# Performance work log

Hardware: AMD Instinct MI355X
Metric: run time of the kernel (lower is better)

## Reference

```python
import jax, jax.numpy as jnp
import numpy as np

IN_CH = 256
OUT_CH = 256
LATENT = 512
SCALE = 1.0 / IN_CH ** 0.5


def setup_inputs() -> dict:
    key = jax.random.key(0)
    k1, k2, k3, k4 = jax.random.split(key, 4)
    return {
        "x": jax.random.normal(k1, (16, IN_CH, 64, 64), dtype=jnp.float32),
        "w": jax.random.normal(k2, (16, LATENT), dtype=jnp.float32),
        "style_w": jax.random.normal(k3, (IN_CH, LATENT), dtype=jnp.float32) * (1.0 / LATENT ** 0.5),
        "style_b": jnp.zeros((IN_CH,), dtype=jnp.float32),
        "weight": jax.random.normal(k4, (1, OUT_CH, IN_CH, 3, 3), dtype=jnp.float32),
    }


def reference(x, w, style_w, style_b, weight):
    b, c, h, ws = x.shape
    # style = Linear(latent -> in_channels), reshaped to [b,1,in,1,1]
    style = (w @ style_w.T + style_b)[:, None, :, None, None]
    wt = weight * SCALE                    # [1, O, I, 3, 3]
    wt = wt * (style + 1.0)                # [b, O, I, 3, 3]
    demod = jax.lax.rsqrt(jnp.sum(wt * wt, axis=(2, 3, 4), keepdims=True) + 1e-8)
    wt = wt * demod
    # grouped conv: fold batch into channels, groups = b
    x2 = x.reshape(1, b * c, h, ws)
    k = wt.reshape(b * OUT_CH, c, 3, 3)
    out = jax.lax.conv_general_dilated(
        x2, k,
        window_strides=(1, 1),
        padding=((1, 1), (1, 1)),
        dimension_numbers=("NCHW", "OIHW", "NCHW"),
        feature_group_count=b,
    )
    return out.reshape(b, OUT_CH, h, ws)
```

## Files before the change

### kernel.cpp

```cpp
#include <hip/hip_runtime.h>
#include <hip/hip_bf16.h>

#define IN_CH 256
#define OUT_CH 256
#define LATENT 512
#define MSCALE (1.0f / 16.0f)

typedef __attribute__((ext_vector_type(8)))  short bf16x8;
typedef __attribute__((ext_vector_type(16))) float f32x16;
typedef unsigned short u16;

__device__ __forceinline__ u16 f2bf(float f) {
  unsigned int x = __float_as_uint(f);
  x += 0x7fffu + ((x >> 16) & 1u);
  return (u16)(x >> 16);
}

__device__ __forceinline__ void gload_lds16(const u16* g, u16* l) {
#if defined(__has_builtin) && __has_builtin(__builtin_amdgcn_global_load_lds)
  __builtin_amdgcn_global_load_lds(
      (const __attribute__((address_space(1))) unsigned int*)g,
      (__attribute__((address_space(3))) unsigned int*)l, 16, 0, 0);
#else
  int lane = __builtin_amdgcn_mbcnt_hi(~0u, __builtin_amdgcn_mbcnt_lo(~0u, 0));
  ((uint4*)l)[lane] = *(const uint4*)g;
#endif
}

__global__ void k_style_demod(const float* __restrict__ w, const float* __restrict__ sw,
                              const float* __restrict__ sb, const float* __restrict__ wsq,
                              float* __restrict__ mod, float* __restrict__ demod) {
  __shared__ float ws[LATENT];
  __shared__ float m2[IN_CH];
  const int b = blockIdx.x, tid = threadIdx.x;
  ws[tid] = w[b * LATENT + tid];
  ws[tid + 256] = w[b * LATENT + 256 + tid];
  __syncthreads();
  const float4* sr = (const float4*)(sw + (size_t)tid * LATENT);
  const float4* wr = (const float4*)ws;
  float s = 0.f;
#pragma unroll 8
  for (int l = 0; l < LATENT / 4; ++l) {
    float4 a = sr[l], c = wr[l];
    s += a.x * c.x + a.y * c.y + a.z * c.z + a.w * c.w;
  }
  float m = (1.0f + s + sb[tid]) * MSCALE;
  mod[b * IN_CH + tid] = m;
  m2[tid] = m * m;
  __syncthreads();
  float acc = 1e-8f;
  const float* q = wsq + (size_t)tid * IN_CH;
#pragma unroll 4
  for (int i = 0; i < IN_CH; ++i) acc += m2[i] * q[i];
  demod[b * OUT_CH + tid] = rsqrtf(acc);
}

__global__ void k_wsq(const float* __restrict__ weight, float* __restrict__ wsq,
                      u16* __restrict__ wb) {
  const int o = blockIdx.x, i = threadIdx.x;
  const float* wp = weight + ((size_t)o * IN_CH + i) * 9;
  float s = 0.f;
#pragma unroll
  for (int t = 0; t < 9; ++t) {
    float v = wp[t];
    s += v * v;
    wb[(((size_t)t * 32 + (i >> 3)) * OUT_CH + o) * 8 + (i & 7)] = f2bf(v);
  }
  wsq[o * IN_CH + i] = s;
}

__global__ __launch_bounds__(256, 2)
void k_conv(const float* __restrict__ x, const u16* __restrict__ wb,
            const float* __restrict__ mod, const float* __restrict__ demod,
            float* __restrict__ out) {
  __shared__ __align__(16) u16 xlds[2 * 10 * 2 * 66 * 8];
  __shared__ __align__(16) u16 wlds[2 * 9 * 2 * 64 * 8];
  __shared__ __align__(16) float modsh[IN_CH];

  const int tid = threadIdx.x;
  const int lane = tid & 63;
  const int wid = tid >> 6;
  const int ol = lane & 31;
  const int hi = lane >> 5;

  const int bid = blockIdx.x;
  const int sbid = ((bid & 7) << 6) | (bid >> 3);
  const int otile = (sbid & 3) << 6;
  const int hbase = ((sbid >> 2) & 7) << 3;
  const int b = sbid >> 5;

  const int sg = (tid >> 6) & 1;
  const int sc1 = tid & 63;
  const int rhalf = tid >> 7;
  const float* xb = x + (size_t)b * 1048576 + sg * 8 * 4096 + sc1;

  int woff[4];
#pragma unroll
  for (int it = 0; it < 4; ++it) {
    int p = it * 256 + tid;
    int t = p >> 7, g = (p >> 6) & 1, o = p & 63;
    woff[it] = ((t * 32 + g) * OUT_CH + otile + o) * 8;
  }
  const int wofft = ((8 * 32 + ((tid >> 6) & 1)) * OUT_CH + otile + (tid & 63)) * 8;

  float mv[8];
  auto ldmod = [&](int ib) {
    float4 m0 = *(const float4*)(modsh + ib + sg * 8);
    float4 m1 = *(const float4*)(modsh + ib + sg * 8 + 4);
    mv[0] = m0.x; mv[1] = m0.y; mv[2] = m0.z; mv[3] = m0.w;
    mv[4] = m1.x; mv[5] = m1.y; mv[6] = m1.z; mv[7] = m1.w;
  };
  auto issueX = [&](int k, int ib, float* v) {
    const int pr = hbase + 2 * k + rhalf;
    const int hc = min(max(pr - 1, 0), 63);
    const float* p = xb + hc * 64 + (size_t)ib * 4096;
#pragma unroll
    for (int j = 0; j < 8; ++j) v[j] = p[(size_t)j * 4096];
  };
  auto commitX = [&](int k, u16* xd, const float* v) {
    const int pr = hbase + 2 * k + rhalf;
    const bool vr = (pr >= 1) && (pr <= 64);
    bf16x8 q;
#pragma unroll
    for (int j = 0; j < 8; ++j) q[j] = vr ? (short)f2bf(v[j] * mv[j]) : (short)0;
    *(bf16x8*)(xd + (size_t)(((2 * k + rhalf) * 2 + sg) * 66 + sc1 + 1) * 8) = q;
  };
  auto stageW = [&](int ibw, u16* wd) {
#pragma unroll
    for (int it = 0; it < 4; ++it)
      gload_lds16(wb + woff[it] + ibw, wd + (size_t)(it * 256 + wid * 64) * 8);
    if (tid < 128)
      gload_lds16(wb + wofft + ibw, wd + (size_t)(1024 + wid * 64) * 8);
  };

  f32x16 acc[2][4] = {};

  modsh[tid] = mod[b * IN_CH + tid];
  if (tid < 80) {
    const int q = tid;
    const int bufz = q / 40, rem = q - bufz * 40;
    const int r = rem >> 2, g = (rem >> 1) & 1, ce = (rem & 1) * 65;
    bf16x8 z = {};
    *(bf16x8*)(xlds + (size_t)(bufz * 1320 + (r * 2 + g) * 66 + ce) * 8) = z;
  }
  __syncthreads();

  {
    float v0[8], v1[8];
    ldmod(0);
    stageW(0, wlds);
    issueX(0, 0, v0); issueX(1, 0, v1);
    commitX(0, xlds, v0); issueX(2, 0, v0);
    commitX(1, xlds, v1); issueX(3, 0, v1);
    commitX(2, xlds, v0); issueX(4, 0, v0);
    commitX(3, xlds, v1);
    commitX(4, xlds, v0);
  }
  __syncthreads();

  for (int ic = 0; ic < 16; ++ic) {
    const int buf = ic & 1;
    const u16* xp = xlds + buf * 10560;
    const u16* wp = wlds + buf * 9216;
    u16* xd = xlds + (buf ^ 1) * 10560;
    u16* wd = wlds + (buf ^ 1) * 9216;
    const bool pf = (ic < 15);
    const int ib = (ic + 1) << 4;

    float v0[8], v1[8];
    if (pf) {
      ldmod(ib);
      stageW((ic + 1) * 4096, wd);
      issueX(0, ib, v0);
      issueX(1, ib, v1);
    }

#pragma unroll
    for (int dh = 0; dh < 3; ++dh) {
      bf16x8 A0[3], A1[3];
#pragma unroll
      for (int dw = 0; dw < 3; ++dw) {
        const int t = dh * 3 + dw;
        A0[dw] = *(const bf16x8*)(wp + (size_t)((t * 2 + hi) * 64 + ol) * 8);
        A1[dw] = *(const bf16x8*)(wp + (size_t)((t * 2 + hi) * 64 + 32 + ol) * 8);
      }
      __builtin_amdgcn_s_setprio(1);
#pragma unroll
      for (int dw = 0; dw < 3; ++dw) {
#pragma unroll
        for (int ps = 0; ps < 4; ++ps) {
          const int r = 2 * wid + (ps >> 1) + dh;
          const int c = (ps & 1) * 32 + ol + dw;
          bf16x8 B = *(const bf16x8*)(xp + (size_t)((r * 2 + hi) * 66 + c) * 8);
          acc[0][ps] = __builtin_amdgcn_mfma_f32_32x32x16_bf16(A0[dw], B, acc[0][ps], 0, 0, 0);
          acc[1][ps] = __builtin_amdgcn_mfma_f32_32x32x16_bf16(A1[dw], B, acc[1][ps], 0, 0, 0);
        }
      }
      __builtin_amdgcn_s_setprio(0);
      if (pf) {
        if (dh == 0) {
          commitX(0, xd, v0); issueX(2, ib, v0);
          commitX(1, xd, v1); issueX(3, ib, v1);
        } else if (dh == 1) {
          commitX(2, xd, v0); issueX(4, ib, v0);
          commitX(3, xd, v1);
        } else {
          commitX(4, xd, v0);
        }
      }
    }
    __syncthreads();
  }

  const float* dmb = demod + b * OUT_CH + otile;
  float* outb = out + (size_t)b * OUT_CH * 4096;
#pragma unroll
  for (int os = 0; os < 2; ++os) {
    float dm[16];
#pragma unroll
    for (int qd = 0; qd < 4; ++qd) {
      float4 d4 = *(const float4*)(dmb + os * 32 + qd * 8 + hi * 4);
      dm[qd * 4 + 0] = d4.x; dm[qd * 4 + 1] = d4.y;
      dm[qd * 4 + 2] = d4.z; dm[qd * 4 + 3] = d4.w;
    }
#pragma unroll
    for (int ps = 0; ps < 4; ++ps) {
      const int prow = hbase + 2 * wid + (ps >> 1);
      const int col = (ps & 1) * 32 + ol;
#pragma unroll
      for (int rr = 0; rr < 16; ++rr) {
        const int orow = (rr & 3) + 8 * (rr >> 2) + 4 * hi;
        const int o = otile + os * 32 + orow;
        outb[(size_t)o * 4096 + prow * 64 + col] = acc[os][ps][rr] * dm[rr];
      }
    }
  }
}

extern "C" void kernel_launch(void* const* d_in, const int* in_sizes, int n_in,
                              void* d_out, int out_size, void* d_ws, size_t ws_size,
                              hipStream_t stream) {
  const float* x  = (const float*)d_in[0];
  const float* w  = (const float*)d_in[1];
  const float* sw = (const float*)d_in[2];
  const float* sb = (const float*)d_in[3];
  const float* wt = (const float*)d_in[4];
  float* out = (float*)d_out;

  char* ws = (char*)d_ws;
  u16*   wbuf  = (u16*)(ws);
  float* mod   = (float*)(ws + 1179648);
  float* demod = (float*)(ws + 1196032);
  float* wsq   = (float*)(ws + 1212416);
  if (ws_size < 1474560u) return;

  k_wsq        <<<256, 256, 0, stream>>>(wt, wsq, wbuf);
  k_style_demod<<<16, 256, 0, stream>>>(w, sw, sb, wsq, mod, demod);
  k_conv       <<<512, 256, 0, stream>>>(x, wbuf, mod, demod, out);
}
```

Before: 113.5 us.

## Merge prep kernels, compute demod in conv, batch x prefetch, packed bf16 convert

The two preprocessing kernels (weight square-sum and bf16 repack, plus the style linear) become one launch. The demodulation reduction moves into the conv kernel, where 64 threads compute it per block into shared memory. This removes a kernel launch and the serial dependency between them. The conv main loop now issues all five x row loads up front and commits them after the MFMA block, and uses the hardware packed bf16 convert instruction. Holding 40 prefetch floats per thread raises register pressure, which could limit occupancy. Each block also recomputes demod redundantly.

New measurement: 102.2 us. -10.0%, faster.

```diff
diff --git a/kernel.cpp b/kernel.cpp
--- a/kernel.cpp
+++ b/kernel.cpp
@@ -9,11 +9,18 @@
 typedef __attribute__((ext_vector_type(8)))  short bf16x8;
 typedef __attribute__((ext_vector_type(16))) float f32x16;
 typedef unsigned short u16;
+typedef unsigned int u32;
 
 __device__ __forceinline__ u16 f2bf(float f) {
   unsigned int x = __float_as_uint(f);
   x += 0x7fffu + ((x >> 16) & 1u);
   return (u16)(x >> 16);
+}
+
+__device__ __forceinline__ u32 pkbf(float lo, float hi) {
+  u32 r;
+  asm("v_cvt_pk_bf16_f32 %0, %1, %2" : "=v"(r) : "v"(lo), "v"(hi));
+  return r;
 }
 
 __device__ __forceinline__ void gload_lds16(const u16* g, u16* l) {
@@ -27,55 +34,48 @@
 #endif
 }
 
-__global__ void k_style_demod(const float* __restrict__ w, const float* __restrict__ sw,
-                              const float* __restrict__ sb, const float* __restrict__ wsq,
-                              float* __restrict__ mod, float* __restrict__ demod) {
-  __shared__ float ws[LATENT];
-  __shared__ float m2[IN_CH];
-  const int b = blockIdx.x, tid = threadIdx.x;
-  ws[tid] = w[b * LATENT + tid];
-  ws[tid + 256] = w[b * LATENT + 256 + tid];
-  __syncthreads();
-  const float4* sr = (const float4*)(sw + (size_t)tid * LATENT);
-  const float4* wr = (const float4*)ws;
-  float s = 0.f;
+__global__ void k_prep(const float* __restrict__ weight, const float* __restrict__ w,
+                       const float* __restrict__ sw, const float* __restrict__ sb,
+                       float* __restrict__ wsq, u16* __restrict__ wb,
+                       float* __restrict__ mod) {
+  const int bid = blockIdx.x, tid = threadIdx.x;
+  if (bid < 256) {
+    const int o = bid, i = tid;
+    const float* wp = weight + ((size_t)o * IN_CH + i) * 9;
+    float s = 0.f;
+#pragma unroll
+    for (int t = 0; t < 9; ++t) {
+      float v = wp[t];
+      s += v * v;
+      wb[(((size_t)t * 32 + (i >> 3)) * OUT_CH + o) * 8 + (i & 7)] = f2bf(v);
+    }
+    wsq[o * IN_CH + i] = s;
+  } else {
+    __shared__ float ws[LATENT];
+    const int b = bid - 256;
+    ws[tid] = w[b * LATENT + tid];
+    ws[tid + 256] = w[b * LATENT + 256 + tid];
+    __syncthreads();
+    const float4* sr = (const float4*)(sw + (size_t)tid * LATENT);
+    const float4* wr = (const float4*)ws;
+    float s = 0.f;
 #pragma unroll 8
-  for (int l = 0; l < LATENT / 4; ++l) {
-    float4 a = sr[l], c = wr[l];
-    s += a.x * c.x + a.y * c.y + a.z * c.z + a.w * c.w;
-  }
-  float m = (1.0f + s + sb[tid]) * MSCALE;
-  mod[b * IN_CH + tid] = m;
-  m2[tid] = m * m;
-  __syncthreads();
-  float acc = 1e-8f;
-  const float* q = wsq + (size_t)tid * IN_CH;
-#pragma unroll 4
-  for (int i = 0; i < IN_CH; ++i) acc += m2[i] * q[i];
-  demod[b * OUT_CH + tid] = rsqrtf(acc);
-}
-
-__global__ void k_wsq(const float* __restrict__ weight, float* __restrict__ wsq,
-                      u16* __restrict__ wb) {
-  const int o = blockIdx.x, i = threadIdx.x;
-  const float* wp = weight + ((size_t)o * IN_CH + i) * 9;
-  float s = 0.f;
-#pragma unroll
-  for (int t = 0; t < 9; ++t) {
-    float v = wp[t];
-    s += v * v;
-    wb[(((size_t)t * 32 + (i >> 3)) * OUT_CH + o) * 8 + (i & 7)] = f2bf(v);
-  }
-  wsq[o * IN_CH + i] = s;
+    for (int l = 0; l < LATENT / 4; ++l) {
+      float4 a = sr[l], c = wr[l];
+      s += a.x * c.x + a.y * c.y + a.z * c.z + a.w * c.w;
+    }
+    mod[b * IN_CH + tid] = (1.0f + s + sb[tid]) * MSCALE;
+  }
 }
 
 __global__ __launch_bounds__(256, 2)
 void k_conv(const float* __restrict__ x, const u16* __restrict__ wb,
-            const float* __restrict__ mod, const float* __restrict__ demod,
+            const float* __restrict__ mod, const float* __restrict__ wsq,
             float* __restrict__ out) {
   __shared__ __align__(16) u16 xlds[2 * 10 * 2 * 66 * 8];
   __shared__ __align__(16) u16 wlds[2 * 9 * 2 * 64 * 8];
   __shared__ __align__(16) float modsh[IN_CH];
+  __shared__ __align__(16) float dmsh[64];
 
   const int tid = threadIdx.x;
   const int lane = tid & 63;
@@ -103,12 +103,13 @@
   }
   const int wofft = ((8 * 32 + ((tid >> 6) & 1)) * OUT_CH + otile + (tid & 63)) * 8;
 
-  float mv[8];
+  float va[5][8];
+  float mvv[8];
   auto ldmod = [&](int ib) {
     float4 m0 = *(const float4*)(modsh + ib + sg * 8);
     float4 m1 = *(const float4*)(modsh + ib + sg * 8 + 4);
-    mv[0] = m0.x; mv[1] = m0.y; mv[2] = m0.z; mv[3] = m0.w;
-    mv[4] = m1.x; mv[5] = m1.y; mv[6] = m1.z; mv[7] = m1.w;
+    mvv[0] = m0.x; mvv[1] = m0.y; mvv[2] = m0.z; mvv[3] = m0.w;
+    mvv[4] = m1.x; mvv[5] = m1.y; mvv[6] = m1.z; mvv[7] = m1.w;
   };
   auto issueX = [&](int k, int ib, float* v) {
     const int pr = hbase + 2 * k + rhalf;
@@ -120,10 +121,12 @@
   auto commitX = [&](int k, u16* xd, const float* v) {
     const int pr = hbase + 2 * k + rhalf;
     const bool vr = (pr >= 1) && (pr <= 64);
-    bf16x8 q;
-#pragma unroll
-    for (int j = 0; j < 8; ++j) q[j] = vr ? (short)f2bf(v[j] * mv[j]) : (short)0;
-    *(bf16x8*)(xd + (size_t)(((2 * k + rhalf) * 2 + sg) * 66 + sc1 + 1) * 8) = q;
+    uint4 q;
+    q.x = vr ? pkbf(v[0] * mvv[0], v[1] * mvv[1]) : 0u;
+    q.y = vr ? pkbf(v[2] * mvv[2], v[3] * mvv[3]) : 0u;
+    q.z = vr ? pkbf(v[4] * mvv[4], v[5] * mvv[5]) : 0u;
+    q.w = vr ? pkbf(v[6] * mvv[6], v[7] * mvv[7]) : 0u;
+    *(uint4*)(xd + (size_t)(((2 * k + rhalf) * 2 + sg) * 66 + sc1 + 1) * 8) = q;
   };
   auto stageW = [&](int ibw, u16* wd) {
 #pragma unroll
@@ -143,19 +146,26 @@
     bf16x8 z = {};
     *(bf16x8*)(xlds + (size_t)(bufz * 1320 + (r * 2 + g) * 66 + ce) * 8) = z;
   }
+#pragma unroll
+  for (int k = 0; k < 5; ++k) issueX(k, 0, va[k]);
+  stageW(0, wlds);
   __syncthreads();
 
-  {
-    float v0[8], v1[8];
-    ldmod(0);
-    stageW(0, wlds);
-    issueX(0, 0, v0); issueX(1, 0, v1);
-    commitX(0, xlds, v0); issueX(2, 0, v0);
-    commitX(1, xlds, v1); issueX(3, 0, v1);
-    commitX(2, xlds, v0); issueX(4, 0, v0);
-    commitX(3, xlds, v1);
-    commitX(4, xlds, v0);
-  }
+  if (tid < 64) {
+    const int o = otile + tid;
+    const float4* wr = (const float4*)(wsq + (size_t)o * IN_CH);
+    const float4* mq = (const float4*)modsh;
+    float s = 1e-8f;
+#pragma unroll 4
+    for (int i = 0; i < IN_CH / 4; ++i) {
+      float4 a = wr[i], c = mq[i];
+      s += a.x * (c.x * c.x) + a.y * (c.y * c.y) + a.z * (c.z * c.z) + a.w * (c.w * c.w);
+    }
+    dmsh[tid] = rsqrtf(s);
+  }
+  ldmod(0);
+#pragma unroll
+  for (int k = 0; k < 5; ++k) commitX(k, xlds, va[k]);
   __syncthreads();
 
   for (int ic = 0; ic < 16; ++ic) {
@@ -167,59 +177,47 @@
     const bool pf = (ic < 15);
     const int ib = (ic + 1) << 4;
 
-    float v0[8], v1[8];
     if (pf) {
       ldmod(ib);
+#pragma unroll
+      for (int k = 0; k < 5; ++k) issueX(k, ib, va[k]);
       stageW((ic + 1) * 4096, wd);
-      issueX(0, ib, v0);
-      issueX(1, ib, v1);
-    }
-
+    }
+
+    __builtin_amdgcn_s_setprio(1);
 #pragma unroll
     for (int dh = 0; dh < 3; ++dh) {
-      bf16x8 A0[3], A1[3];
 #pragma unroll
       for (int dw = 0; dw < 3; ++dw) {
         const int t = dh * 3 + dw;
-        A0[dw] = *(const bf16x8*)(wp + (size_t)((t * 2 + hi) * 64 + ol) * 8);
-        A1[dw] = *(const bf16x8*)(wp + (size_t)((t * 2 + hi) * 64 + 32 + ol) * 8);
-      }
-      __builtin_amdgcn_s_setprio(1);
-#pragma unroll
-      for (int dw = 0; dw < 3; ++dw) {
+        bf16x8 A0 = *(const bf16x8*)(wp + (size_t)((t * 2 + hi) * 64 + ol) * 8);
+        bf16x8 A1 = *(const bf16x8*)(wp + (size_t)((t * 2 + hi) * 64 + 32 + ol) * 8);
 #pragma unroll
         for (int ps = 0; ps < 4; ++ps) {
           const int r = 2 * wid + (ps >> 1) + dh;
           const int c = (ps & 1) * 32 + ol + dw;
           bf16x8 B = *(const bf16x8*)(xp + (size_t)((r * 2 + hi) * 66 + c) * 8);
-          acc[0][ps] = __builtin_amdgcn_mfma_f32_32x32x16_bf16(A0[dw], B, acc[0][ps], 0, 0, 0);
-          acc[1][ps] = __builtin_amdgcn_mfma_f32_32x32x16_bf16(A1[dw], B, acc[1][ps], 0, 0, 0);
+          acc[0][ps] = __builtin_amdgcn_mfma_f32_32x32x16_bf16(A0, B, acc[0][ps], 0, 0, 0);
+          acc[1][ps] = __builtin_amdgcn_mfma_f32_32x32x16_bf16(A1, B, acc[1][ps], 0, 0, 0);
         }
       }
-      __builtin_amdgcn_s_setprio(0);
-      if (pf) {
-        if (dh == 0) {
-          commitX(0, xd, v0); issueX(2, ib, v0);
-          commitX(1, xd, v1); issueX(3, ib, v1);
-        } else if (dh == 1) {
-          commitX(2, xd, v0); issueX(4, ib, v0);
-          commitX(3, xd, v1);
-        } else {
-          commitX(4, xd, v0);
-        }
-      }
+    }
+    __builtin_amdgcn_s_setprio(0);
+
+    if (pf) {
+#pragma unroll
+      for (int k = 0; k < 5; ++k) commitX(k, xd, va[k]);
     }
     __syncthreads();
   }
 
-  const float* dmb = demod + b * OUT_CH + otile;
   float* outb = out + (size_t)b * OUT_CH * 4096;
 #pragma unroll
   for (int os = 0; os < 2; ++os) {
     float dm[16];
 #pragma unroll
     for (int qd = 0; qd < 4; ++qd) {
-      float4 d4 = *(const float4*)(dmb + os * 32 + qd * 8 + hi * 4);
+      float4 d4 = *(const float4*)(dmsh + os * 32 + qd * 8 + hi * 4);
       dm[qd * 4 + 0] = d4.x; dm[qd * 4 + 1] = d4.y;
       dm[qd * 4 + 2] = d4.z; dm[qd * 4 + 3] = d4.w;
     }
@@ -250,11 +248,9 @@
   char* ws = (char*)d_ws;
   u16*   wbuf  = (u16*)(ws);
   float* mod   = (float*)(ws + 1179648);
-  float* demod = (float*)(ws + 1196032);
-  float* wsq   = (float*)(ws + 1212416);
-  if (ws_size < 1474560u) return;
-
-  k_wsq        <<<256, 256, 0, stream>>>(wt, wsq, wbuf);
-  k_style_demod<<<16, 256, 0, stream>>>(w, sw, sb, wsq, mod, demod);
-  k_conv       <<<512, 256, 0, stream>>>(x, wbuf, mod, demod, out);
-}
+  float* wsq   = (float*)(ws + 1196032);
+  if (ws_size < 1458176u) return;
+
+  k_prep<<<272, 256, 0, stream>>>(wt, w, sw, sb, wsq, wbuf, mod);
+  k_conv<<<512, 256, 0, stream>>>(x, wbuf, mod, wsq, out);
+}
```
